# Optimization experiments

Hardware: AMD Instinct MI355X
Metric: run time of the kernel (lower is better)

## Reference

```python
import jax, jax.numpy as jnp
import numpy as np

DIAG_FLOOR = 0.1
DIAG_CEIL = 1.0


def setup_inputs() -> dict:
    key = jax.random.key(0)
    k1, k2, k3, k4 = jax.random.split(key, 4)
    m, in_f, out_f = 16384, 1024, 2048
    z = jax.random.normal(k1, (m, in_f), dtype=jnp.float32)
    diag_params = jax.random.normal(k2, (out_f, in_f), dtype=jnp.float32)
    mean_params = 5.0 * jax.random.normal(k3, (out_f, in_f, 1), dtype=jnp.float32)
    scale_params = jax.random.normal(k4, (out_f,), dtype=jnp.float32)
    return {"z": z, "diag_params": diag_params, "mean_params": mean_params,
            "scale_params": scale_params}


def reference(z, diag_params, mean_params, scale_params):
    # Clamp diag to (0.1, 1.0) via sigmoid; clamp scale via tanh.
    d = DIAG_FLOOR + (DIAG_CEIL - DIAG_FLOOR) * jax.nn.sigmoid(diag_params)  # (out, in)
    mean = mean_params[..., 0]  # (out, in)

    # Diagonal covariance => quadratic forms reduce to elementwise products:
    # z_cov_z[m,k]    = sum_i d[k,i] * z[m,i]^2
    # mean_cov_mean[k]= sum_i d[k,i] * mean[k,i]^2
    # z_cov_mean[m,k] = sum_i z[m,i] * d[k,i] * mean[k,i]
    z_cov_z = jnp.einsum('mi,ki->mk', z * z, d)          # (m, out)
    mean_cov_mean = jnp.sum(d * mean * mean, axis=1)      # (out,)
    z_cov_mean = jnp.einsum('mi,ki->mk', z, d * mean)     # (m, out)

    scaling = jnp.tanh(scale_params)                      # (out,)
    return scaling * jnp.exp(-z_cov_z - mean_cov_mean + 2.0 * z_cov_mean)
```

## Files before the change

kernel.cpp:

```cpp
#include <hip/hip_runtime.h>
#include <hip/hip_bf16.h>
#include <cstdint>
#include <cstddef>

#define M_DIM 16384
#define IN_F  1024
#define OUT_F 2048
#define K_CAT 2048
#define NT    (K_CAT / 32)

typedef float f32x16 __attribute__((ext_vector_type(16)));
typedef short short8 __attribute__((ext_vector_type(8)));

__device__ __forceinline__ void gld_lds16(const void* gptr, void* lptr) {
    __builtin_amdgcn_global_load_lds(
        (const __attribute__((address_space(1))) uint32_t*)gptr,
        (__attribute__((address_space(3))) uint32_t*)lptr,
        16 , 0 , 0 );
}

__global__ __launch_bounds__(256) void prep_z_kernel(const float* __restrict__ z,
                                                     __hip_bfloat16* __restrict__ A) {
    const int idx = blockIdx.x * 256 + threadIdx.x;
    const int m  = idx >> 7;
    const int c8 = (idx & 127) * 8;
    const float4 v0 = ((const float4*)z)[idx * 2];
    const float4 v1 = ((const float4*)z)[idx * 2 + 1];
    const float x[8] = {v0.x, v0.y, v0.z, v0.w, v1.x, v1.y, v1.z, v1.w};
    __hip_bfloat16 q[8], r[8];
#pragma unroll
    for (int j = 0; j < 8; ++j) {
        q[j] = __float2bfloat16(x[j] * x[j]);
        r[j] = __float2bfloat16(x[j]);
    }
    __hip_bfloat16* rowp = A + (size_t)m * K_CAT;
    *(uint4*)&rowp[c8]        = *(uint4*)q;
    *(uint4*)&rowp[IN_F + c8] = *(uint4*)r;
}

__global__ __launch_bounds__(256) void prep_b_kernel(const float* __restrict__ diag,
                                                     const float* __restrict__ mean,
                                                     const float* __restrict__ scale,
                                                     __hip_bfloat16* __restrict__ B,
                                                     float* __restrict__ mcm,
                                                     float* __restrict__ ts) {
    const int k = blockIdx.x;
    const int t = threadIdx.x;
    const float4 dp = ((const float4*)(diag + (size_t)k * IN_F))[t];
    const float4 mp = ((const float4*)(mean + (size_t)k * IN_F))[t];
    const float dx[4] = {dp.x, dp.y, dp.z, dp.w};
    const float mx[4] = {mp.x, mp.y, mp.z, mp.w};
    __hip_bfloat16 nb[4], pb[4];
    float acc = 0.f;
#pragma unroll
    for (int j = 0; j < 4; ++j) {
        const float d = 0.1f + 0.9f / (1.f + __expf(-dx[j]));
        nb[j] = __float2bfloat16(-d);
        pb[j] = __float2bfloat16(2.f * d * mx[j]);
        acc += d * mx[j] * mx[j];
    }
    __hip_bfloat16* rowp = B + (size_t)k * K_CAT;
    *(uint2*)&rowp[t * 4]        = *(uint2*)nb;
    *(uint2*)&rowp[IN_F + t * 4] = *(uint2*)pb;
#pragma unroll
    for (int off = 32; off > 0; off >>= 1) acc += __shfl_down(acc, off);
    __shared__ float red[4];
    if ((t & 63) == 0) red[t >> 6] = acc;
    __syncthreads();
    if (t == 0) {
        mcm[k] = red[0] + red[1] + red[2] + red[3];
        ts[k]  = tanhf(scale[k]);
    }
}

__global__ __launch_bounds__(512, 2) void gemm_exp_kernel(
    const __hip_bfloat16* __restrict__ A,
    const __hip_bfloat16* __restrict__ B,
    const float* __restrict__ mcm,
    const float* __restrict__ ts,
    float* __restrict__ out) {
    __shared__ __align__(16) __hip_bfloat16 smem[4][2][8192];

    const int t = threadIdx.x;
    const int wg = ((blockIdx.x & 7) << 6) | (blockIdx.x >> 3);
    const int tn = wg & 7;
    const int tm = wg >> 3;

    const int c0 = t, c1 = t + 512;
    const int r0 = c0 >> 2, u0 = c0 & 3;
    const int r1 = c1 >> 2, u1 = c1 & 3;
    const int s0 = u0 ^ ((r0 >> 1) & 3);
    const int s1 = u1 ^ ((r1 >> 1) & 3);
    const __hip_bfloat16* gA0 = A + (size_t)(tm * 256 + r0) * K_CAT + s0 * 8;
    const __hip_bfloat16* gA1 = A + (size_t)(tm * 256 + r1) * K_CAT + s1 * 8;
    const __hip_bfloat16* gB0 = B + (size_t)(tn * 256 + r0) * K_CAT + s0 * 8;
    const __hip_bfloat16* gB1 = B + (size_t)(tn * 256 + r1) * K_CAT + s1 * 8;

#define ISSUE_A(buf_, kt_) do { \
        gld_lds16(gA0 + (kt_) * 32, &smem[buf_][0][c0 * 8]); \
        gld_lds16(gA1 + (kt_) * 32, &smem[buf_][0][c1 * 8]); } while (0)
#define ISSUE_B(buf_, kt_) do { \
        gld_lds16(gB0 + (kt_) * 32, &smem[buf_][1][c0 * 8]); \
        gld_lds16(gB1 + (kt_) * 32, &smem[buf_][1][c1 * 8]); } while (0)

    const int wid = t >> 6, lane = t & 63;
    const int wmb = (wid >> 2) * 128;
    const int wnb = (wid & 3) * 64;
    const int l31 = lane & 31, lh = lane >> 5;
    int offA[4][2], offB[2][2];
#pragma unroll
    for (int fm = 0; fm < 4; ++fm) {
        const int r = wmb + fm * 32 + l31;
#pragma unroll
        for (int ks = 0; ks < 2; ++ks) {
            const int slot = 2 * ks + lh;
            offA[fm][ks] = r * 32 + (slot ^ ((r >> 1) & 3)) * 8;
        }
    }
#pragma unroll
    for (int fn = 0; fn < 2; ++fn) {
        const int r = wnb + fn * 32 + l31;
#pragma unroll
        for (int ks = 0; ks < 2; ++ks) {
            const int slot = 2 * ks + lh;
            offB[fn][ks] = r * 32 + (slot ^ ((r >> 1) & 3)) * 8;
        }
    }

    f32x16 acc[4][2] = {};

    ISSUE_A(0, 0); ISSUE_B(0, 0);
    ISSUE_A(1, 1); ISSUE_B(1, 1);
    ISSUE_A(2, 2); ISSUE_B(2, 2);
    asm volatile("s_waitcnt vmcnt(16)" ::: "memory");
    __builtin_amdgcn_s_barrier();
    __builtin_amdgcn_sched_barrier(0);

#pragma unroll 4
    for (int kt = 0; kt < NT; ++kt) {
        const int buf  = kt & 3;
        const int pf   = (kt < NT - 3) ? kt + 3 : NT - 1;
        const int pbuf = (kt + 3) & 3;

        short8 a0[4], a1[4], b0[2], b1[2];
#pragma unroll
        for (int fm = 0; fm < 4; ++fm) a0[fm] = *(const short8*)&smem[buf][0][offA[fm][0]];
#pragma unroll
        for (int fn = 0; fn < 2; ++fn) b0[fn] = *(const short8*)&smem[buf][1][offB[fn][0]];
        __builtin_amdgcn_sched_barrier(0);
#pragma unroll
        for (int fm = 0; fm < 4; ++fm) a1[fm] = *(const short8*)&smem[buf][0][offA[fm][1]];
#pragma unroll
        for (int fn = 0; fn < 2; ++fn) b1[fn] = *(const short8*)&smem[buf][1][offB[fn][1]];
        ISSUE_A(pbuf, pf);
        ISSUE_B(pbuf, pf);
        __builtin_amdgcn_sched_barrier(0);
        asm volatile("s_waitcnt lgkmcnt(6)" ::: "memory");
        __builtin_amdgcn_sched_barrier(0);
        __builtin_amdgcn_s_setprio(1);
#pragma unroll
        for (int fm = 0; fm < 4; ++fm)
#pragma unroll
            for (int fn = 0; fn < 2; ++fn)
                acc[fm][fn] = __builtin_amdgcn_mfma_f32_32x32x16_bf16(
                    a0[fm], b0[fn], acc[fm][fn], 0, 0, 0);
        __builtin_amdgcn_s_setprio(0);
        __builtin_amdgcn_sched_barrier(0);
        asm volatile("s_waitcnt lgkmcnt(0)" ::: "memory");
        __builtin_amdgcn_sched_barrier(0);
        __builtin_amdgcn_s_setprio(1);
#pragma unroll
        for (int fm = 0; fm < 4; ++fm)
#pragma unroll
            for (int fn = 0; fn < 2; ++fn)
                acc[fm][fn] = __builtin_amdgcn_mfma_f32_32x32x16_bf16(
                    a1[fm], b1[fn], acc[fm][fn], 0, 0, 0);
        __builtin_amdgcn_s_setprio(0);
        __builtin_amdgcn_sched_barrier(0);
        asm volatile("s_waitcnt vmcnt(16)" ::: "memory");
        __builtin_amdgcn_s_barrier();
        __builtin_amdgcn_sched_barrier(0);
    }
#undef ISSUE_A
#undef ISSUE_B

#pragma unroll
    for (int fn = 0; fn < 2; ++fn) {
        const int gn = tn * 256 + wnb + fn * 32 + l31;
        const float tsv = ts[gn];
        const float mv  = mcm[gn];
#pragma unroll
        for (int fm = 0; fm < 4; ++fm) {
            const int gm0 = tm * 256 + wmb + fm * 32 + lh * 4;
#pragma unroll
            for (int reg = 0; reg < 16; ++reg) {
                const int row = (reg & 3) + 8 * (reg >> 2);
                out[(size_t)(gm0 + row) * OUT_F + gn] = tsv * __expf(acc[fm][fn][reg] - mv);
            }
        }
    }
}

extern "C" void kernel_launch(void* const* d_in, const int* in_sizes, int n_in,
                              void* d_out, int out_size, void* d_ws, size_t ws_size,
                              hipStream_t stream) {
    const float* z     = (const float*)d_in[0];
    const float* diag  = (const float*)d_in[1];
    const float* mean  = (const float*)d_in[2];
    const float* scale = (const float*)d_in[3];
    float* out = (float*)d_out;

    char* ws = (char*)d_ws;
    const size_t A_BYTES = (size_t)M_DIM * K_CAT * sizeof(__hip_bfloat16);
    const size_t B_BYTES = (size_t)OUT_F * K_CAT * sizeof(__hip_bfloat16);
    __hip_bfloat16* Abuf = (__hip_bfloat16*)ws;
    __hip_bfloat16* Bbuf = (__hip_bfloat16*)(ws + A_BYTES);
    float* mcm = (float*)(ws + A_BYTES + B_BYTES);
    float* ts  = (float*)(ws + A_BYTES + B_BYTES + 8192);

    prep_z_kernel<<<(M_DIM * IN_F / 8) / 256, 256, 0, stream>>>(z, Abuf);
    prep_b_kernel<<<OUT_F, 256, 0, stream>>>(diag, mean, scale, Bbuf, mcm, ts);
    gemm_exp_kernel<<<(M_DIM / 256) * (OUT_F / 256), 512, 0, stream>>>(
        Abuf, Bbuf, mcm, ts, out);
}
```

Before: 326.5 us.

## Double-buffer A fragments in registers and prefetch next k-tile during MFMAs

```diff
diff --git a/kernel.cpp b/kernel.cpp
--- a/kernel.cpp
+++ b/kernel.cpp
@@ -128,59 +128,56 @@
     }
 
     f32x16 acc[4][2] = {};
+    short8 aE[4][2], aO[4][2];
 
     ISSUE_A(0, 0); ISSUE_B(0, 0);
     ISSUE_A(1, 1); ISSUE_B(1, 1);
     ISSUE_A(2, 2); ISSUE_B(2, 2);
-    asm volatile("s_waitcnt vmcnt(16)" ::: "memory");
+    asm volatile("s_waitcnt vmcnt(8)" ::: "memory");
     __builtin_amdgcn_s_barrier();
     __builtin_amdgcn_sched_barrier(0);
-
-#pragma unroll 4
-    for (int kt = 0; kt < NT; ++kt) {
-        const int buf  = kt & 3;
-        const int pf   = (kt < NT - 3) ? kt + 3 : NT - 1;
-        const int pbuf = (kt + 3) & 3;
-
-        short8 a0[4], a1[4], b0[2], b1[2];
-#pragma unroll
-        for (int fm = 0; fm < 4; ++fm) a0[fm] = *(const short8*)&smem[buf][0][offA[fm][0]];
-#pragma unroll
-        for (int fn = 0; fn < 2; ++fn) b0[fn] = *(const short8*)&smem[buf][1][offB[fn][0]];
-        __builtin_amdgcn_sched_barrier(0);
-#pragma unroll
-        for (int fm = 0; fm < 4; ++fm) a1[fm] = *(const short8*)&smem[buf][0][offA[fm][1]];
-#pragma unroll
-        for (int fn = 0; fn < 2; ++fn) b1[fn] = *(const short8*)&smem[buf][1][offB[fn][1]];
-        ISSUE_A(pbuf, pf);
-        ISSUE_B(pbuf, pf);
-        __builtin_amdgcn_sched_barrier(0);
-        asm volatile("s_waitcnt lgkmcnt(6)" ::: "memory");
-        __builtin_amdgcn_sched_barrier(0);
-        __builtin_amdgcn_s_setprio(1);
-#pragma unroll
-        for (int fm = 0; fm < 4; ++fm)
-#pragma unroll
-            for (int fn = 0; fn < 2; ++fn)
-                acc[fm][fn] = __builtin_amdgcn_mfma_f32_32x32x16_bf16(
-                    a0[fm], b0[fn], acc[fm][fn], 0, 0, 0);
-        __builtin_amdgcn_s_setprio(0);
-        __builtin_amdgcn_sched_barrier(0);
-        asm volatile("s_waitcnt lgkmcnt(0)" ::: "memory");
-        __builtin_amdgcn_sched_barrier(0);
-        __builtin_amdgcn_s_setprio(1);
-#pragma unroll
-        for (int fm = 0; fm < 4; ++fm)
-#pragma unroll
-            for (int fn = 0; fn < 2; ++fn)
-                acc[fm][fn] = __builtin_amdgcn_mfma_f32_32x32x16_bf16(
-                    a1[fm], b1[fn], acc[fm][fn], 0, 0, 0);
-        __builtin_amdgcn_s_setprio(0);
-        __builtin_amdgcn_sched_barrier(0);
-        asm volatile("s_waitcnt vmcnt(16)" ::: "memory");
-        __builtin_amdgcn_s_barrier();
-        __builtin_amdgcn_sched_barrier(0);
-    }
+#pragma unroll
+    for (int fm = 0; fm < 4; ++fm)
+#pragma unroll
+        for (int ks = 0; ks < 2; ++ks)
+            aE[fm][ks] = *(const short8*)&smem[0][0][offA[fm][ks]];
+    asm volatile("s_waitcnt lgkmcnt(0)" ::: "memory");
+    __builtin_amdgcn_sched_barrier(0);
+
+#define SUBITER(KT_, ACUR_, ANXT_) do {                                        \
+    const int pf_   = ((KT_) + 3 < NT) ? (KT_) + 3 : NT - 1;                   \
+    const int pbuf_ = ((KT_) + 3) & 3;                                         \
+    ISSUE_A(pbuf_, pf_); ISSUE_B(pbuf_, pf_);                                  \
+    __builtin_amdgcn_sched_barrier(0);                                         \
+    short8 bc_[2][2];                                                          \
+    _Pragma("unroll") for (int fn = 0; fn < 2; ++fn)                           \
+        _Pragma("unroll") for (int ks = 0; ks < 2; ++ks)                       \
+            bc_[fn][ks] = *(const short8*)&smem[(KT_) & 3][1][offB[fn][ks]];   \
+    __builtin_amdgcn_sched_barrier(0);         \
+    _Pragma("unroll") for (int fm = 0; fm < 4; ++fm)                           \
+        _Pragma("unroll") for (int ks = 0; ks < 2; ++ks)                       \
+            ANXT_[fm][ks] = *(const short8*)&smem[((KT_) + 1) & 3][0][offA[fm][ks]]; \
+    __builtin_amdgcn_sched_barrier(0);                                         \
+    asm volatile("s_waitcnt lgkmcnt(8)" ::: "memory");           \
+    __builtin_amdgcn_sched_barrier(0);                                         \
+    __builtin_amdgcn_s_setprio(1);                                             \
+    _Pragma("unroll") for (int ks = 0; ks < 2; ++ks)                           \
+        _Pragma("unroll") for (int fm = 0; fm < 4; ++fm)                       \
+            _Pragma("unroll") for (int fn = 0; fn < 2; ++fn)                   \
+                acc[fm][fn] = __builtin_amdgcn_mfma_f32_32x32x16_bf16(         \
+                    ACUR_[fm][ks], bc_[fn][ks], acc[fm][fn], 0, 0, 0);         \
+    __builtin_amdgcn_s_setprio(0);                                             \
+    __builtin_amdgcn_sched_barrier(0);                                         \
+    asm volatile("s_waitcnt vmcnt(4)" ::: "memory");    \
+    __builtin_amdgcn_s_barrier();                                              \
+    __builtin_amdgcn_sched_barrier(0);                                         \
+} while (0)
+
+    for (int kt = 0; kt < NT; kt += 2) {
+        SUBITER(kt,     aE, aO);
+        SUBITER(kt + 1, aO, aE);
+    }
+#undef SUBITER
 #undef ISSUE_A
 #undef ISSUE_B
 
```

New measurement: 330.7 us. No clear change (+1.3%).
